# Kernel optimization log

Measured on AMD Instinct MI355X. Metric: run time of the kernel, lower is better.

The kernel has to match this reference:

```python
import jax, jax.numpy as jnp
import numpy as np

H = 16        # num query heads
HKV = 4       # num kv heads
D = 128       # head_dim
HID = 2048    # hidden_size
G = H // HKV  # heads per kv group


def setup_inputs() -> dict:
    key = jax.random.key(0)
    ks = jax.random.split(key, 9)
    s = 0.02
    x = jax.random.normal(ks[0], (2, 2048, HID), dtype=jnp.float32)
    wq = jax.random.normal(ks[1], (HID, H * D), dtype=jnp.float32) * s
    bq = jnp.zeros((H * D,), jnp.float32)
    wk = jax.random.normal(ks[2], (HID, HKV * D), dtype=jnp.float32) * s
    bk = jnp.zeros((HKV * D,), jnp.float32)
    wv = jax.random.normal(ks[3], (HID, HKV * D), dtype=jnp.float32) * s
    bv = jnp.zeros((HKV * D,), jnp.float32)
    wo = jax.random.normal(ks[4], (HID, HID), dtype=jnp.float32) * s
    bo = jnp.zeros((HID,), jnp.float32)
    return dict(x=x, wq=wq, bq=bq, wk=wk, bk=bk, wv=wv, bv=bv, wo=wo, bo=bo)


def reference(x, wq, bq, wk, bk, wv, bv, wo, bo):
    B, S, _ = x.shape
    scale = jnp.float32(1.0 / np.sqrt(D))
    # projections (torch Linear with weight stored as [in, out] here)
    q = (x @ wq + bq).reshape(B, S, H, D)          # [B,S,H,D]
    k = (x @ wk + bk).reshape(B, S, HKV, D)        # [B,S,Hkv,D]
    v = (x @ wv + bv).reshape(B, S, HKV, D)
    # group query heads by kv head instead of expanding KV
    q = q.reshape(B, S, HKV, G, D)
    scores = jnp.einsum('bqhgd,bkhd->bhgqk', q, k) * scale  # [B,Hkv,G,S,S]
    causal = jnp.triu(jnp.ones((S, S), dtype=bool), k=1)
    scores = jnp.where(causal, jnp.float32(-1e9), scores)
    weights = jax.nn.softmax(scores, axis=-1)
    out = jnp.einsum('bhgqk,bkhd->bqhgd', weights, v)        # [B,S,Hkv,G,D]
    out = out.reshape(B, S, H * D)
    return out @ wo + bo
```

## Files before the change

kernel.cpp:

```cpp
#include <hip/hip_runtime.h>
#include <hip/hip_bf16.h>
#include <math.h>

#define HID 2048
#define NH 16
#define NKV 4
#define HD 128
#define GQ 4
#define BATCH 2

typedef short short8v __attribute__((ext_vector_type(8)));
typedef float f32x4 __attribute__((ext_vector_type(4)));

__device__ __forceinline__ ushort f2bf(float f) {
  uint u = __float_as_uint(f);
  uint r = (u + 0x7fffu + ((u >> 16) & 1u)) >> 16;
  return (ushort)r;
}

__device__ __forceinline__ uint cvt_pk_bf16(float lo, float hi) {
  uint r;
  asm("v_cvt_pk_bf16_f32 %0, %1, %2" : "=v"(r) : "v"(lo), "v"(hi));
  return r;
}

__device__ __forceinline__ void gld_lds16(const void* g, void* lds) {
  __builtin_amdgcn_global_load_lds(
      (const __attribute__((address_space(1))) unsigned int*)g,
      (__attribute__((address_space(3))) unsigned int*)lds, 16, 0, 0);
}

#define WAVE_LDS_FENCE()                                \
  do {                                                  \
    asm volatile("s_waitcnt lgkmcnt(0)" ::: "memory");  \
    __builtin_amdgcn_sched_barrier(0);                  \
  } while (0)

__device__ const int QT_TAB[24] = {7, 8, 9, 10, 11, 12, 13, 14, 15, 15, 6, 14,
                                   5, 13, 4, 12, 3, 11, 2, 10, 1, 9, 0, 8};
__device__ const int LO_TAB[24] = {0, 0, 0, 0, 0, 0, 0, 0, 0, 16, 0, 16,
                                   0, 16, 0, 16, 0, 16, 0, 16, 0, 16, 0, 16};

__global__ __launch_bounds__(256) void prep_kernel(
    const float* __restrict__ x, ushort* __restrict__ xb,
    const float* __restrict__ wq, ushort* __restrict__ wqT,
    const float* __restrict__ wk, ushort* __restrict__ wkT,
    const float* __restrict__ wv, ushort* __restrict__ wvT,
    const float* __restrict__ wo, ushort* __restrict__ woT) {
  const int bid = blockIdx.x;
  const int t = threadIdx.x;
  if (bid < 4096) {
    const int i = (bid * 256 + t) * 8;
    float4 f0 = *reinterpret_cast<const float4*>(x + i);
    float4 f1 = *reinterpret_cast<const float4*>(x + i + 4);
    uint4 o;
    o.x = (uint)f2bf(f0.x) | ((uint)f2bf(f0.y) << 16);
    o.y = (uint)f2bf(f0.z) | ((uint)f2bf(f0.w) << 16);
    o.z = (uint)f2bf(f1.x) | ((uint)f2bf(f1.y) << 16);
    o.w = (uint)f2bf(f1.z) | ((uint)f2bf(f1.w) << 16);
    *reinterpret_cast<uint4*>(xb + i) = o;
  } else {
    const float* W;
    ushort* Wt;
    int N, idx;
    if (bid < 8192)       { W = wq; Wt = wqT; N = 2048; idx = bid - 4096; }
    else if (bid < 9216)  { W = wk; Wt = wkT; N = 512;  idx = bid - 8192; }
    else if (bid < 10240) { W = wv; Wt = wvT; N = 512;  idx = bid - 9216; }
    else                  { W = wo; Wt = woT; N = 2048; idx = bid - 10240; }
    const int K = 2048;
    const int k0 = (idx & 63) * 32;
    const int n0 = (idx >> 6) * 32;
    __shared__ float T[32][33];
    const int r = t >> 3;
    const int c4 = (t & 7) * 4;
    float4 vin = *reinterpret_cast<const float4*>(
        &W[(size_t)(k0 + r) * N + n0 + c4]);
    T[c4 + 0][r] = vin.x;
    T[c4 + 1][r] = vin.y;
    T[c4 + 2][r] = vin.z;
    T[c4 + 3][r] = vin.w;
    __syncthreads();
    ushort4 o;
    o.x = f2bf(T[r][c4 + 0]);
    o.y = f2bf(T[r][c4 + 1]);
    o.z = f2bf(T[r][c4 + 2]);
    o.w = f2bf(T[r][c4 + 3]);
    *reinterpret_cast<ushort4*>(&Wt[(size_t)(n0 + r) * K + k0 + c4]) = o;
  }
}

__global__ __launch_bounds__(256) void merge_kernel(
    const float* __restrict__ OaccA, const float* __restrict__ OaccB,
    const float* __restrict__ LaccA, const float* __restrict__ LaccB,
    ushort* __restrict__ attnb) {
  const int i = (int)blockIdx.x * 256 + (int)threadIdx.x;
  const int d8 = i & 15;
  const int h = (i >> 4) & 15;
  const int r = i >> 8;
  const float invl = 1.0f / (LaccA[r * NH + h] + LaccB[r * NH + h]);
  const size_t off = ((size_t)r * (NH * HD)) + h * HD + d8 * 8;
  float4 a0 = *reinterpret_cast<const float4*>(OaccA + off);
  float4 a1 = *reinterpret_cast<const float4*>(OaccA + off + 4);
  float4 b0 = *reinterpret_cast<const float4*>(OaccB + off);
  float4 b1 = *reinterpret_cast<const float4*>(OaccB + off + 4);
  uint4 o;
  o.x = cvt_pk_bf16((a0.x + b0.x) * invl, (a0.y + b0.y) * invl);
  o.y = cvt_pk_bf16((a0.z + b0.z) * invl, (a0.w + b0.w) * invl);
  o.z = cvt_pk_bf16((a1.x + b1.x) * invl, (a1.y + b1.y) * invl);
  o.w = cvt_pk_bf16((a1.z + b1.z) * invl, (a1.w + b1.w) * invl);
  const int b = r >> 10;
  const int s = 1024 + (r & 1023);
  *reinterpret_cast<uint4*>(
      &attnb[((size_t)(b * 2048 + s)) * (NH * HD) + h * HD + d8 * 8]) = o;
}

template <int MODE>
__global__ __launch_bounds__(512, 2) void gemm_big(
    const ushort* __restrict__ A,
    const ushort* __restrict__ W0, const ushort* __restrict__ W1,
    const ushort* __restrict__ W2,
    const float* __restrict__ b0, const float* __restrict__ b1,
    const float* __restrict__ b2,
    void* __restrict__ C0, void* __restrict__ C1, void* __restrict__ C2,
    int M, int K, int S) {
  __shared__ ushort As[3][256 * 32];
  __shared__ ushort Bs[3][256 * 32];
  const int tid = threadIdx.x;

  const int nbx = (int)gridDim.x;
  int bid = (int)blockIdx.y * nbx + (int)blockIdx.x;
  const int cpx = (nbx * (int)gridDim.y) >> 3;
  bid = (bid & 7) * cpx + (bid >> 3);
  const int m0 = (bid / nbx) * 256;
  const int n0 = (bid % nbx) * 256;

  const int wave = tid >> 6;
  const int lane = tid & 63;
  const int quad = lane >> 4;
  const int lr = lane & 15;
  const int l4 = lane >> 2;
  const int lcs = ((lane & 3) ^ ((lane >> 3) & 3)) * 8;
  const int cswz = (quad ^ ((lr >> 1) & 3)) * 8;
  const int wm = (wave >> 1) * 64;
  const int wn = (wave & 1) * 128;

  const ushort* Wt;
  const float* bias;
  int nloc, Nout, om;
  void* Cout;
  if (MODE == 0) {
    Wt = W0; bias = b0; nloc = n0; Nout = 2048; om = 0; Cout = C0;
  } else {
    if (n0 < 2048)      { Wt = W0; bias = b0; nloc = n0;        Nout = 2048; om = 1; Cout = C0; }
    else if (n0 < 2560) { Wt = W1; bias = b1; nloc = n0 - 2048; Nout = 512;  om = 1; Cout = C1; }
    else                { Wt = W2; bias = b2; nloc = n0 - 2560; Nout = 512;  om = 2; Cout = C2; }
  }

  f32x4 acc[4][8];
#pragma unroll
  for (int i = 0; i < 4; ++i)
#pragma unroll
    for (int j = 0; j < 8; ++j) acc[i][j] = (f32x4){0.f, 0.f, 0.f, 0.f};

  const size_t rowA = (size_t)(m0 + wave * 32 + l4) * K + lcs;
  const size_t rowB = (size_t)(nloc + wave * 32 + l4) * K + lcs;

#define STAGE_GEMM(t, bi)                                                  \
  do {                                                                     \
    const int kof = (t) * 32;                                              \
    gld_lds16(&A[rowA + kof], &As[bi][(wave * 32) * 32]);                  \
    gld_lds16(&A[rowA + 16 * K + kof], &As[bi][(wave * 32 + 16) * 32]);    \
    gld_lds16(&Wt[rowB + kof], &Bs[bi][(wave * 32) * 32]);                 \
    gld_lds16(&Wt[rowB + 16 * K + kof], &Bs[bi][(wave * 32 + 16) * 32]);   \
  } while (0)

  const int nt = K / 32;
  STAGE_GEMM(0, 0);
  STAGE_GEMM(1, 1);

  for (int t = 0; t < nt; ++t) {
    const int cur = t % 3;
    __builtin_amdgcn_s_barrier();
    if (t + 2 < nt) {
      STAGE_GEMM(t + 2, (t + 2) % 3);
      asm volatile("s_waitcnt vmcnt(8)" ::: "memory");
    } else if (t + 1 < nt) {
      asm volatile("s_waitcnt vmcnt(4)" ::: "memory");
    } else {
      asm volatile("s_waitcnt vmcnt(0)" ::: "memory");
    }
    __builtin_amdgcn_s_barrier();
    __builtin_amdgcn_sched_barrier(0);

    short8v af[4], bf[8];
#pragma unroll
    for (int x = 0; x < 4; ++x) {
      const int ra = wm + x * 16 + lr;
      af[x] = *reinterpret_cast<const short8v*>(&As[cur][ra * 32 + cswz]);
    }
#pragma unroll
    for (int y = 0; y < 8; ++y) {
      const int rb = wn + y * 16 + lr;
      bf[y] = *reinterpret_cast<const short8v*>(&Bs[cur][rb * 32 + cswz]);
    }
#pragma unroll
    for (int i = 0; i < 4; ++i)
#pragma unroll
      for (int j = 0; j < 8; ++j)
        acc[i][j] = __builtin_amdgcn_mfma_f32_16x16x32_bf16(
            af[i], bf[j], acc[i][j], 0, 0, 0);
  }
#undef STAGE_GEMM

#pragma unroll
  for (int i = 0; i < 4; ++i) {
    const int row_base = m0 + wm + i * 16 + quad * 4;
#pragma unroll
    for (int j = 0; j < 8; ++j) {
      const int col = nloc + wn + j * 16 + lr;
      const float b = bias[col];
      if (om == 0) {
        float* C = (float*)Cout;
#pragma unroll
        for (int rg = 0; rg < 4; ++rg)
          C[(size_t)(row_base + rg) * Nout + col] = acc[i][j][rg] + b;
      } else if (om == 1) {
        ushort* C = (ushort*)Cout;
#pragma unroll
        for (int rg = 0; rg < 4; ++rg)
          C[(size_t)(row_base + rg) * Nout + col] = f2bf(acc[i][j][rg] + b);
      } else {
        ushort* C = (ushort*)Cout;
        const int bb = (row_base >= S) ? 1 : 0;
        const int s = row_base - bb * S;
        const int kvh = col >> 7;
        const int d = col & 127;
        ushort4 o;
        o.x = f2bf(acc[i][j][0] + b);
        o.y = f2bf(acc[i][j][1] + b);
        o.z = f2bf(acc[i][j][2] + b);
        o.w = f2bf(acc[i][j][3] + b);
        *reinterpret_cast<ushort4*>(
            &C[((size_t)(bb * NKV + kvh) * HD + d) * S + s]) = o;
      }
    }
  }
}

__device__ __forceinline__ void stage_k8(const ushort* __restrict__ Kb,
                                         ushort* Kdst, int k0, int wave,
                                         int lane) {
  const int rK = lane >> 4, cK = lane & 15;
#pragma unroll
  for (int c = 0; c < 2; ++c) {
    const int g = wave * 2 + c;
    const int row = g * 4 + rK;
    const int jk = cK ^ (row & 15);
    gld_lds16(&Kb[(size_t)(k0 + row) * (NKV * HD) + jk * 8], &Kdst[g * 512]);
  }
}
__device__ __forceinline__ void stage_v8(const ushort* __restrict__ Vb,
                                         ushort* Vdst, int k0, int S, int wave,
                                         int lane) {
  const int rV = lane >> 3, cV = lane & 7;
#pragma unroll
  for (int c = 0; c < 2; ++c) {
    const int g = wave * 2 + c;
    const int d = g * 8 + rV;
    const int jv = cV ^ (d & 7);
    gld_lds16(&Vb[(size_t)d * S + k0 + jv * 8], &Vdst[g * 512]);
  }
}

__global__ __launch_bounds__(512, 4) void gqa_attn_mfma(
    const ushort* __restrict__ Qg, const ushort* __restrict__ Kgl,
    const ushort* __restrict__ Vt_g, ushort* __restrict__ O,
    float* __restrict__ OaccA, float* __restrict__ OaccB,
    float* __restrict__ LaccA, float* __restrict__ LaccB, int S) {
  __shared__ __align__(16) ushort L[24576];
  ushort* K0 = L;
  ushort* K1 = L + 8192;
  ushort* Vs = L + 16384;

  const int tid = threadIdx.x;
  const int wave = tid >> 6;
  const int lane = tid & 63;
  const int quad = lane >> 4;
  const int lr = lane & 15;
  const int item = blockIdx.z;
  const int qt = QT_TAB[item];
  const int lo = LO_TAB[item];
  const int ntf = 2 * qt + 2;
  const int hi = lo ? ntf : (ntf < 16 ? ntf : 16);
  const bool part = (qt >= 8);
  const int q0 = qt * 128;
  const int hq = blockIdx.x;
  const int b = blockIdx.y;
  const int kvh = hq >> 2;
  const float C = 0.12751745f;

  const ushort* Qb = Qg + ((size_t)b * S) * (NH * HD) + (size_t)hq * HD;
  const ushort* Kb = Kgl + ((size_t)b * S) * (NKV * HD) + (size_t)kvh * HD;
  const ushort* Vb = Vt_g + ((size_t)(b * NKV + kvh) * HD) * S;

#pragma unroll
  for (int i = 0; i < 4; ++i) {
    const int id = tid + i * 512;
    const int r = id >> 4, c = id & 15;
    const int p = c ^ (r & 15);
    *reinterpret_cast<uint4*>(&L[r * 128 + p * 8]) =
        *reinterpret_cast<const uint4*>(
            &Qb[(size_t)(q0 + r) * (NH * HD) + c * 8]);
  }
  __syncthreads();
  short8v aq[4];
  {
    const int ra = wave * 16 + lr;
#pragma unroll
    for (int ks = 0; ks < 4; ++ks)
      aq[ks] = *reinterpret_cast<const short8v*>(
          &L[ra * 128 + (((ks * 4 + quad) ^ lr) & 15) * 8]);
  }
  __syncthreads();

  f32x4 oacc[8];
#pragma unroll
  for (int nb = 0; nb < 8; ++nb) oacc[nb] = (f32x4){0.f, 0.f, 0.f, 0.f};
  float l_r = 0.f;

  const int laneA = ((quad * 2) & 3) * 16 + lr;
  const int laneB = ((quad * 2 + 1) & 3) * 16 + lr;
  const bool hihalf = (quad >= 2);

  stage_k8(Kb, (lo & 1) ? K1 : K0, lo * 64, wave, lane);

  for (int kt = lo; kt < hi; ++kt) {
    const int k0v = kt * 64;
    const ushort* Kc = (kt & 1) ? K1 : K0;

    __builtin_amdgcn_s_barrier();
    stage_v8(Vb, Vs, k0v, S, wave, lane);
    if (kt + 1 < hi) {
      stage_k8(Kb, (kt & 1) ? K0 : K1, k0v + 64, wave, lane);
      asm volatile("s_waitcnt vmcnt(4)" ::: "memory");
    } else {
      asm volatile("s_waitcnt vmcnt(2)" ::: "memory");
    }
    __builtin_amdgcn_s_barrier();
    __builtin_amdgcn_sched_barrier(0);

    f32x4 sacc[4];
    __builtin_amdgcn_s_setprio(1);
#pragma unroll
    for (int nb = 0; nb < 4; ++nb) {
      sacc[nb] = (f32x4){0.f, 0.f, 0.f, 0.f};
      const int rb = nb * 16 + lr;
#pragma unroll
      for (int ks = 0; ks < 4; ++ks) {
        short8v bk = *reinterpret_cast<const short8v*>(
            &Kc[rb * 128 + (((ks * 4 + quad) ^ lr) & 15) * 8]);
        sacc[nb] = __builtin_amdgcn_mfma_f32_16x16x32_bf16(
            bk, aq[ks], sacc[nb], 0, 0, 0);
      }
    }
    __builtin_amdgcn_s_setprio(0);

    const bool needmask = (kt >= 2 * qt);
    const int qi = q0 + wave * 16 + lr;
    uint u[4][2];
    float rs = 0.f;
#pragma unroll
    for (int nb = 0; nb < 4; ++nb) {
      float p[4];
#pragma unroll
      for (int rg = 0; rg < 4; ++rg) {
        float sv = sacc[nb][rg] * C;
        if (needmask) {
          const int kj = k0v + nb * 16 + quad * 4 + rg;
          if (kj > qi) sv = -1e30f;
        }
        p[rg] = __builtin_amdgcn_exp2f(sv);
        rs += p[rg];
      }
      u[nb][0] = cvt_pk_bf16(p[0], p[1]);
      u[nb][1] = cvt_pk_bf16(p[2], p[3]);
    }
    rs += __shfl_xor(rs, 16);
    rs += __shfl_xor(rs, 32);
    l_r += rs;

    short8v ap[2];
#pragma unroll
    for (int ks = 0; ks < 2; ++ks) {
      const uint w0a = __shfl(u[2 * ks + 0][0], laneA);
      const uint w0b = __shfl(u[2 * ks + 1][0], laneA);
      const uint w1a = __shfl(u[2 * ks + 0][1], laneA);
      const uint w1b = __shfl(u[2 * ks + 1][1], laneA);
      const uint w2a = __shfl(u[2 * ks + 0][0], laneB);
      const uint w2b = __shfl(u[2 * ks + 1][0], laneB);
      const uint w3a = __shfl(u[2 * ks + 0][1], laneB);
      const uint w3b = __shfl(u[2 * ks + 1][1], laneB);
      uint4 q4;
      q4.x = hihalf ? w0b : w0a;
      q4.y = hihalf ? w1b : w1a;
      q4.z = hihalf ? w2b : w2a;
      q4.w = hihalf ? w3b : w3a;
      ap[ks] = *reinterpret_cast<short8v*>(&q4);
    }

    if (kt + 1 < hi) {
      asm volatile("s_waitcnt vmcnt(2)" ::: "memory");
    } else {
      asm volatile("s_waitcnt vmcnt(0)" ::: "memory");
    }
    __builtin_amdgcn_s_barrier();
    __builtin_amdgcn_sched_barrier(0);

    __builtin_amdgcn_s_setprio(1);
#pragma unroll
    for (int nb = 0; nb < 8; ++nb) {
      const int rv = nb * 16 + lr;
#pragma unroll
      for (int ks = 0; ks < 2; ++ks) {
        short8v bv = *reinterpret_cast<const short8v*>(
            &Vs[rv * 64 + (((ks * 4 + quad) ^ lr) & 7) * 8]);
        oacc[nb] = __builtin_amdgcn_mfma_f32_16x16x32_bf16(
            ap[ks], bv, oacc[nb], 0, 0, 0);
      }
    }
    __builtin_amdgcn_s_setprio(0);
  }

  if (part) {
    float* Oacc = lo ? OaccB : OaccA;
    float* Lacc = lo ? LaccB : LaccA;
    float* Oa = Oacc +
                ((size_t)(b * 1024 + (q0 - 1024) + wave * 16 + quad * 4)) *
                    (NH * HD) +
                hq * HD;
#pragma unroll
    for (int nb = 0; nb < 8; ++nb)
#pragma unroll
      for (int rg = 0; rg < 4; ++rg)
        Oa[(size_t)rg * (NH * HD) + nb * 16 + lr] = oacc[nb][rg];
    if (quad == 0)
      Lacc[(size_t)(b * 1024 + (q0 - 1024) + wave * 16 + lr) * NH + hq] = l_r;
  } else {
    const float invl = 1.0f / l_r;
    float inv[4];
#pragma unroll
    for (int rg = 0; rg < 4; ++rg)
      inv[rg] = __shfl(invl, (lane & 48) | (quad * 4 + rg));
    __syncthreads();
    ushort* ow = &L[wave * 16 * 128];
#pragma unroll
    for (int nb = 0; nb < 8; ++nb)
#pragma unroll
      for (int rg = 0; rg < 4; ++rg)
        ow[(quad * 4 + rg) * 128 + nb * 16 + lr] =
            f2bf(oacc[nb][rg] * inv[rg]);
    WAVE_LDS_FENCE();
    ushort* Ob = O + ((size_t)b * S) * (NH * HD) + (size_t)hq * HD;
#pragma unroll
    for (int ii = 0; ii < 4; ++ii) {
      const int id = lane + ii * 64;
      const int r16 = id >> 4, c = id & 15;
      uint4 val = *reinterpret_cast<const uint4*>(&ow[r16 * 128 + c * 8]);
      *reinterpret_cast<uint4*>(
          &Ob[(size_t)(q0 + wave * 16 + r16) * (NH * HD) + c * 8]) = val;
    }
  }
}

extern "C" void kernel_launch(void* const* d_in, const int* in_sizes, int n_in,
                              void* d_out, int out_size, void* d_ws,
                              size_t ws_size, hipStream_t stream) {
  const float* x = (const float*)d_in[0];
  const float* wq = (const float*)d_in[1];
  const float* bq = (const float*)d_in[2];
  const float* wk = (const float*)d_in[3];
  const float* bk = (const float*)d_in[4];
  const float* wv = (const float*)d_in[5];
  const float* bv = (const float*)d_in[6];
  const float* wo = (const float*)d_in[7];
  const float* bo = (const float*)d_in[8];
  float* out = (float*)d_out;

  const int M = in_sizes[0] / HID;
  const int S = M / BATCH;

  char* w = (char*)d_ws;
  ushort* xb    = (ushort*)(w + 0);
  ushort* qb    = (ushort*)(w + (16u << 20));
  ushort* kb    = (ushort*)(w + (32u << 20));
  ushort* vT    = (ushort*)(w + (36u << 20));
  ushort* attnb = (ushort*)(w + (40u << 20));
  ushort* wqT   = (ushort*)(w + (56u << 20));
  ushort* wkT   = (ushort*)(w + (64u << 20));
  ushort* wvT   = (ushort*)(w + (66u << 20));
  ushort* woT   = (ushort*)(w + (68u << 20));
  float* OaccA = (float*)(w + 0);
  float* OaccB = out;
  float* LaccA = (float*)(w + (64u << 20));
  float* LaccB = (float*)(w + (66u << 20));

  prep_kernel<<<dim3(14336), dim3(256), 0, stream>>>(
      x, xb, wq, wqT, wk, wkT, wv, wvT, wo, woT);

  gemm_big<1><<<dim3(3072 / 256, M / 256), dim3(512), 0, stream>>>(
      xb, wqT, wkT, wvT, bq, bk, bv, qb, kb, vT, M, HID, S);

  gqa_attn_mfma<<<dim3(NH, BATCH, 24), dim3(512), 0, stream>>>(
      qb, kb, vT, attnb, OaccA, OaccB, LaccA, LaccB, S);

  merge_kernel<<<dim3(2048), dim3(256), 0, stream>>>(
      OaccA, OaccB, LaccA, LaccB, attnb);

  gemm_big<0><<<dim3(HID / 256, M / 256), dim3(512), 0, stream>>>(
      attnb, woT, nullptr, nullptr, bo, nullptr, nullptr,
      out, nullptr, nullptr, M, HID, S);
}
```

Measured before the change: 350.0 us.

## Restructure big GEMM into K=64 double-buffered, four-phase interleaved pipeline

The projection/output GEMM kernel moves from a triple-buffered K=32 loop to a double-buffered K=64 tile. Each iteration is split into four phases that interleave LDS fragment loads, quarter-tile global-to-LDS staging, and MFMA bursts under raised wave priority. The wave layout also changes from 4x2 to 2x4, with a new XOR swizzle for 64-wide rows. The aim is to overlap memory staging with MFMA work and halve the per-iteration barrier overhead, at the cost of more barriers per iteration and tighter hand-tuned vmcnt accounting that could be fragile.

```diff
diff --git a/kernel.cpp b/kernel.cpp
--- a/kernel.cpp
+++ b/kernel.cpp
@@ -123,8 +123,8 @@
     const float* __restrict__ b2,
     void* __restrict__ C0, void* __restrict__ C1, void* __restrict__ C2,
     int M, int K, int S) {
-  __shared__ ushort As[3][256 * 32];
-  __shared__ ushort Bs[3][256 * 32];
+  __shared__ ushort As[2][256 * 64];
+  __shared__ ushort Bs[2][256 * 64];
   const int tid = threadIdx.x;
 
   const int nbx = (int)gridDim.x;
@@ -138,11 +138,10 @@
   const int lane = tid & 63;
   const int quad = lane >> 4;
   const int lr = lane & 15;
-  const int l4 = lane >> 2;
-  const int lcs = ((lane & 3) ^ ((lane >> 3) & 3)) * 8;
-  const int cswz = (quad ^ ((lr >> 1) & 3)) * 8;
-  const int wm = (wave >> 1) * 64;
-  const int wn = (wave & 1) * 128;
+  const int wr = wave >> 2;
+  const int wc = wave & 3;
+  const int rloc = lane >> 3;
+  const int gc8 = ((lane & 7) ^ rloc) * 8;
 
   const ushort* Wt;
   const float* bias;
@@ -156,68 +155,124 @@
     else                { Wt = W2; bias = b2; nloc = n0 - 2560; Nout = 512;  om = 2; Cout = C2; }
   }
 
-  f32x4 acc[4][8];
-#pragma unroll
-  for (int i = 0; i < 4; ++i)
-#pragma unroll
-    for (int j = 0; j < 8; ++j) acc[i][j] = (f32x4){0.f, 0.f, 0.f, 0.f};
-
-  const size_t rowA = (size_t)(m0 + wave * 32 + l4) * K + lcs;
-  const size_t rowB = (size_t)(nloc + wave * 32 + l4) * K + lcs;
-
-#define STAGE_GEMM(t, bi)                                                  \
-  do {                                                                     \
-    const int kof = (t) * 32;                                              \
-    gld_lds16(&A[rowA + kof], &As[bi][(wave * 32) * 32]);                  \
-    gld_lds16(&A[rowA + 16 * K + kof], &As[bi][(wave * 32 + 16) * 32]);    \
-    gld_lds16(&Wt[rowB + kof], &Bs[bi][(wave * 32) * 32]);                 \
-    gld_lds16(&Wt[rowB + 16 * K + kof], &Bs[bi][(wave * 32 + 16) * 32]);   \
+  f32x4 acc[8][4];
+#pragma unroll
+  for (int i = 0; i < 8; ++i)
+#pragma unroll
+    for (int j = 0; j < 4; ++j) acc[i][j] = (f32x4){0.f, 0.f, 0.f, 0.f};
+
+  const int nt = K / 64;
+
+#define STAGE_HALF(bf, tt, h)                                               \
+  do {                                                                      \
+    const ushort* s_ = ((h) < 2) ? A : Wt;                                  \
+    const int base_ = ((h) < 2) ? m0 : nloc;                                \
+    ushort* d_ = ((h) < 2) ? &As[bf][0] : &Bs[bf][0];                       \
+    const int hh_ = (h) & 1;                                                \
+    gld_lds16(&s_[(size_t)(base_ + hh_ * 128 + wave * 8 + rloc) * K +       \
+                  (tt) * 64 + gc8],                                         \
+              &d_[hh_ * 8192 + wave * 512]);                                \
+    gld_lds16(&s_[(size_t)(base_ + hh_ * 128 + 64 + wave * 8 + rloc) * K +  \
+                  (tt) * 64 + gc8],                                         \
+              &d_[hh_ * 8192 + 4096 + wave * 512]);                         \
   } while (0)
 
-  const int nt = K / 32;
-  STAGE_GEMM(0, 0);
-  STAGE_GEMM(1, 1);
+#define LOAD_A(qi)                                                          \
+  do {                                                                      \
+    _Pragma("unroll") for (int fi = 0; fi < 4; ++fi)                        \
+        _Pragma("unroll") for (int ks = 0; ks < 2; ++ks) {                  \
+      const int row_ = wr * 128 + (qi)*64 + fi * 16 + lr;                   \
+      afr[fi][ks] = *reinterpret_cast<const short8v*>(                      \
+          &As[cur][row_ * 64 + (((ks * 4 + quad) ^ (lr & 7))) * 8]);        \
+    }                                                                       \
+  } while (0)
+#define LOAD_B(qj)                                                          \
+  do {                                                                      \
+    _Pragma("unroll") for (int fj = 0; fj < 2; ++fj)                        \
+        _Pragma("unroll") for (int ks = 0; ks < 2; ++ks) {                  \
+      const int row_ = wc * 64 + (qj)*32 + fj * 16 + lr;                    \
+      bfr[fj][ks] = *reinterpret_cast<const short8v*>(                      \
+          &Bs[cur][row_ * 64 + (((ks * 4 + quad) ^ (lr & 7))) * 8]);        \
+    }                                                                       \
+  } while (0)
+#define MFMA_Q(qi, qj)                                                      \
+  do {                                                                      \
+    __builtin_amdgcn_s_setprio(1);                                          \
+    _Pragma("unroll") for (int fi = 0; fi < 4; ++fi)                        \
+        _Pragma("unroll") for (int fj = 0; fj < 2; ++fj)                    \
+            _Pragma("unroll") for (int ks = 0; ks < 2; ++ks)                \
+                acc[(qi)*4 + fi][(qj)*2 + fj] =                             \
+        __builtin_amdgcn_mfma_f32_16x16x32_bf16(                            \
+            afr[fi][ks], bfr[fj][ks], acc[(qi)*4 + fi][(qj)*2 + fj], 0, 0,  \
+            0);                                                             \
+    __builtin_amdgcn_s_setprio(0);                                          \
+  } while (0)
+#define PHASE_SYNC()                                    \
+  do {                                                  \
+    __builtin_amdgcn_s_barrier();                       \
+    asm volatile("s_waitcnt lgkmcnt(0)" ::: "memory");  \
+    __builtin_amdgcn_sched_barrier(0);                  \
+  } while (0)
+#define PHASE_END() __builtin_amdgcn_s_barrier()
+
+  STAGE_HALF(0, 0, 0);
+  STAGE_HALF(0, 0, 1);
+  STAGE_HALF(0, 0, 2);
+  STAGE_HALF(0, 0, 3);
+  if (nt > 1) {
+    STAGE_HALF(1, 1, 0);
+    asm volatile("s_waitcnt vmcnt(2)" ::: "memory");
+  } else {
+    asm volatile("s_waitcnt vmcnt(0)" ::: "memory");
+  }
+  __builtin_amdgcn_s_barrier();
 
   for (int t = 0; t < nt; ++t) {
-    const int cur = t % 3;
-    __builtin_amdgcn_s_barrier();
-    if (t + 2 < nt) {
-      STAGE_GEMM(t + 2, (t + 2) % 3);
-      asm volatile("s_waitcnt vmcnt(8)" ::: "memory");
-    } else if (t + 1 < nt) {
-      asm volatile("s_waitcnt vmcnt(4)" ::: "memory");
-    } else {
-      asm volatile("s_waitcnt vmcnt(0)" ::: "memory");
-    }
-    __builtin_amdgcn_s_barrier();
-    __builtin_amdgcn_sched_barrier(0);
-
-    short8v af[4], bf[8];
-#pragma unroll
-    for (int x = 0; x < 4; ++x) {
-      const int ra = wm + x * 16 + lr;
-      af[x] = *reinterpret_cast<const short8v*>(&As[cur][ra * 32 + cswz]);
-    }
-#pragma unroll
-    for (int y = 0; y < 8; ++y) {
-      const int rb = wn + y * 16 + lr;
-      bf[y] = *reinterpret_cast<const short8v*>(&Bs[cur][rb * 32 + cswz]);
-    }
-#pragma unroll
-    for (int i = 0; i < 4; ++i)
-#pragma unroll
-      for (int j = 0; j < 8; ++j)
-        acc[i][j] = __builtin_amdgcn_mfma_f32_16x16x32_bf16(
-            af[i], bf[j], acc[i][j], 0, 0, 0);
-  }
-#undef STAGE_GEMM
-
-#pragma unroll
-  for (int i = 0; i < 4; ++i) {
-    const int row_base = m0 + wm + i * 16 + quad * 4;
-#pragma unroll
-    for (int j = 0; j < 8; ++j) {
-      const int col = nloc + wn + j * 16 + lr;
+    const int cur = t & 1;
+    short8v afr[4][2], bfr[2][2];
+    LOAD_A(0);
+    LOAD_B(0);
+    if (t + 1 < nt) STAGE_HALF(cur ^ 1, t + 1, 1);
+    PHASE_SYNC();
+    MFMA_Q(0, 0);
+    PHASE_END();
+    LOAD_B(1);
+    if (t + 1 < nt) STAGE_HALF(cur ^ 1, t + 1, 2);
+    PHASE_SYNC();
+    MFMA_Q(0, 1);
+    PHASE_END();
+    LOAD_A(1);
+    LOAD_B(0);
+    if (t + 1 < nt) STAGE_HALF(cur ^ 1, t + 1, 3);
+    PHASE_SYNC();
+    MFMA_Q(1, 0);
+    PHASE_END();
+    LOAD_B(1);
+    if (t + 2 < nt) STAGE_HALF(cur, t + 2, 0);
+    if (t + 1 < nt) {
+      if (t + 2 < nt) {
+        asm volatile("s_waitcnt vmcnt(2)" ::: "memory");
+      } else {
+        asm volatile("s_waitcnt vmcnt(0)" ::: "memory");
+      }
+    }
+    PHASE_SYNC();
+    MFMA_Q(1, 1);
+    PHASE_END();
+  }
+#undef STAGE_HALF
+#undef LOAD_A
+#undef LOAD_B
+#undef MFMA_Q
+#undef PHASE_SYNC
+#undef PHASE_END
+
+#pragma unroll
+  for (int i = 0; i < 8; ++i) {
+    const int row_base = m0 + wr * 128 + i * 16 + quad * 4;
+#pragma unroll
+    for (int j = 0; j < 4; ++j) {
+      const int col = nloc + wc * 64 + j * 16 + lr;
       const float b = bias[col];
       if (om == 0) {
         float* C = (float*)Cout;
```

After: 318.9 us. -8.9%, faster.
